# Optimization experiments

Measured on AMD Instinct MI355X. Metric: run time of the kernel, lower is better.

## Reference

```python
import jax, jax.numpy as jnp
import numpy as np

B, DIM, HID = 16384, 1024, 2048


def _ln(x, g, b, eps=1e-5):
    m = x.mean(-1, keepdims=True)
    v = ((x - m) ** 2).mean(-1, keepdims=True)
    return (x - m) / jnp.sqrt(v + eps) * g + b


def _attn1(x_kv, Wv, bv, Wo, bo):
    # seq-len-1 MHA: softmax over a single key is exactly 1 (per head),
    # so output = out_proj(v_proj(kv)); q/k projections cancel identically.
    return (x_kv @ Wv.T + bv) @ Wo.T + bo


def _ffn(x, W1, b1, W2, b2):
    return jnp.maximum(x @ W1.T + b1, 0.0) @ W2.T + b2


def setup_inputs() -> dict:
    key = jax.random.key(0)
    ks = iter(jax.random.split(key, 32))
    s = 0.02
    d = {
        'visual_feat': jax.random.normal(next(ks), (B, DIM), jnp.float32),
        'text_feat': jax.random.normal(next(ks), (B, DIM), jnp.float32),
    }
    for tag in ('sv', 'st', 'v2t', 't2v'):
        d[f'Wv_{tag}'] = jax.random.normal(next(ks), (DIM, DIM), jnp.float32) * s
        d[f'bv_{tag}'] = jnp.zeros((DIM,), jnp.float32)
        d[f'Wo_{tag}'] = jax.random.normal(next(ks), (DIM, DIM), jnp.float32) * s
        d[f'bo_{tag}'] = jnp.zeros((DIM,), jnp.float32)
    for tag in ('v1', 't1', 'v2', 't2'):
        d[f'g_{tag}'] = jnp.ones((DIM,), jnp.float32)
        d[f'be_{tag}'] = jnp.zeros((DIM,), jnp.float32)
    for tag in ('v', 't'):
        d[f'W1_{tag}'] = jax.random.normal(next(ks), (HID, DIM), jnp.float32) * s
        d[f'b1_{tag}'] = jnp.zeros((HID,), jnp.float32)
        d[f'W2_{tag}'] = jax.random.normal(next(ks), (DIM, HID), jnp.float32) * s
        d[f'b2_{tag}'] = jnp.zeros((DIM,), jnp.float32)
    return d


def reference(visual_feat, text_feat,
              Wv_sv, bv_sv, Wo_sv, bo_sv,
              Wv_st, bv_st, Wo_st, bo_st,
              Wv_v2t, bv_v2t, Wo_v2t, bo_v2t,
              Wv_t2v, bv_t2v, Wo_t2v, bo_t2v,
              g_v1, be_v1, g_t1, be_t1, g_v2, be_v2, g_t2, be_t2,
              W1_v, b1_v, W2_v, b2_v, W1_t, b1_t, W2_t, b2_t):
    v_self = _ln(visual_feat + _attn1(visual_feat, Wv_sv, bv_sv, Wo_sv, bo_sv), g_v1, be_v1)
    t_self = _ln(text_feat + _attn1(text_feat, Wv_st, bv_st, Wo_st, bo_st), g_t1, be_t1)
    v_cross = _attn1(t_self, Wv_v2t, bv_v2t, Wo_v2t, bo_v2t)  # v queries t -> depends on kv=t_self only
    t_cross = _attn1(v_self, Wv_t2v, bv_t2v, Wo_t2v, bo_t2v)
    v_fused = _ln(visual_feat + (v_self + v_cross) * 0.5, g_v2, be_v2)
    t_fused = _ln(text_feat + (t_self + t_cross) * 0.5, g_t2, be_t2)
    v_out = v_fused + _ffn(v_fused, W1_v, b1_v, W2_v, b2_v)
    t_out = t_fused + _ffn(t_fused, W1_t, b1_t, W2_t, b2_t)
    new_context = (v_out + t_out) * 0.5
    return (v_out, t_out, new_context)
```

## Files before the change

kernel.cpp:

```cpp
#include <hip/hip_runtime.h>
#include <stdint.h>


typedef unsigned short u16;
typedef __bf16 bf16x8 __attribute__((ext_vector_type(8)));
typedef float f32x4 __attribute__((ext_vector_type(4)));

__device__ __forceinline__ u16 f2bf(float f) {
    uint32_t x = __float_as_uint(f);
    uint32_t r = (x + 0x7fffu + ((x >> 16) & 1u)) >> 16;
    return (u16)r;
}
__device__ __forceinline__ float bf2f(u16 u) {
    return __uint_as_float(((uint32_t)u) << 16);
}

__device__ __forceinline__ void glds16(const u16* g, u16* l) {
    __builtin_amdgcn_global_load_lds(
        (__attribute__((address_space(1))) void*)g,
        (__attribute__((address_space(3))) void*)l, 16, 0, 0);
}

__global__ __launch_bounds__(256) void cvtk(const float* __restrict__ src,
                                            u16* __restrict__ dst) {
    size_t i = ((size_t)blockIdx.x * 256 + threadIdx.x) * 4;
    float4 v = *(const float4*)&src[i];
    ushort4 o;
    o.x = f2bf(v.x); o.y = f2bf(v.y); o.z = f2bf(v.z); o.w = f2bf(v.w);
    *(ushort4*)&dst[i] = o;
}

struct Ptr4 { const float* p[4]; };
__global__ __launch_bounds__(256) void tcvtk(Ptr4 src, u16* __restrict__ dst) {
    __shared__ float t[32][33];
    const int z = blockIdx.z;
    const float* s = src.p[z];
    const int bx = blockIdx.x * 32, by = blockIdx.y * 32;
    const int tx = threadIdx.x & 31, ty = threadIdx.x >> 5;
#pragma unroll
    for (int i = 0; i < 32; i += 8)
        t[ty + i][tx] = s[(size_t)(by + ty + i) * 1024 + bx + tx];
    __syncthreads();
    u16* d = dst + (size_t)z * (1024 * 1024);
#pragma unroll
    for (int i = 0; i < 32; i += 8)
        d[(size_t)(bx + ty + i) * 1024 + by + tx] = f2bf(t[tx][ty + i]);
}

struct BiasArgs { const float* Wo[4]; const float* bv[4]; const float* bo[4]; };
__global__ __launch_bounds__(256) void biask(BiasArgs a, float* __restrict__ out) {
    const int z = blockIdx.y;
    const int row = blockIdx.x * 4 + (threadIdx.x >> 6);
    const int lane = threadIdx.x & 63;
    const float* w = a.Wo[z] + (size_t)row * 1024 + lane * 16;
    const float* v = a.bv[z] + lane * 16;
    float s = 0.f;
#pragma unroll
    for (int i = 0; i < 16; i += 4) {
        float4 w4 = *(const float4*)&w[i];
        float4 v4 = *(const float4*)&v[i];
        s += w4.x * v4.x + w4.y * v4.y + w4.z * v4.z + w4.w * v4.w;
    }
#pragma unroll
    for (int o = 1; o < 64; o <<= 1) s += __shfl_xor(s, o);
    if (lane == 0) out[(size_t)z * 1024 + row] = s + a.bo[z][row];
}

__global__ __launch_bounds__(256) void ctxk(const float* __restrict__ a,
                                            const float* __restrict__ b,
                                            float* __restrict__ o) {
    size_t i = ((size_t)blockIdx.x * 256 + threadIdx.x) * 4;
    float4 va = *(const float4*)&a[i];
    float4 vb = *(const float4*)&b[i];
    float4 vo;
    vo.x = 0.5f * (va.x + vb.x); vo.y = 0.5f * (va.y + vb.y);
    vo.z = 0.5f * (va.z + vb.z); vo.w = 0.5f * (va.w + vb.w);
    *(float4*)&o[i] = vo;
}

__global__ __launch_bounds__(256) void ln_kernel(
    const float* __restrict__ x, const u16* __restrict__ a1,
    const u16* __restrict__ a2, float s,
    const float* __restrict__ g, const float* __restrict__ be,
    u16* __restrict__ out) {
    const int tid = threadIdx.x;
    const size_t base = (size_t)blockIdx.x * 1024;
    const int i0 = tid * 4;

    float4 xv = *(const float4*)&x[base + i0];
    ushort4 u1 = *(const ushort4*)&a1[base + i0];
    float add[4] = {bf2f(u1.x), bf2f(u1.y), bf2f(u1.z), bf2f(u1.w)};
    if (a2) {
        ushort4 u2 = *(const ushort4*)&a2[base + i0];
        add[0] += bf2f(u2.x); add[1] += bf2f(u2.y);
        add[2] += bf2f(u2.z); add[3] += bf2f(u2.w);
    }
    float v[4] = {xv.x, xv.y, xv.z, xv.w};
    float sum = 0.f, ss = 0.f;
#pragma unroll
    for (int j = 0; j < 4; ++j) {
        v[j] += s * add[j];
        sum += v[j];
        ss += v[j] * v[j];
    }
#pragma unroll
    for (int o = 1; o < 64; o <<= 1) {
        sum += __shfl_xor(sum, o);
        ss  += __shfl_xor(ss, o);
    }
    __shared__ float s1[4], s2[4];
    if ((tid & 63) == 0) { s1[tid >> 6] = sum; s2[tid >> 6] = ss; }
    __syncthreads();
    sum = s1[0] + s1[1] + s1[2] + s1[3];
    ss  = s2[0] + s2[1] + s2[2] + s2[3];
    const float mean = sum * (1.f / 1024.f);
    const float var  = ss * (1.f / 1024.f) - mean * mean;
    const float inv  = rsqrtf(var + 1e-5f);

    float4 gv = *(const float4*)&g[i0];
    float4 bv = *(const float4*)&be[i0];
    ushort4 o4;
    o4.x = f2bf((v[0] - mean) * inv * gv.x + bv.x);
    o4.y = f2bf((v[1] - mean) * inv * gv.y + bv.y);
    o4.z = f2bf((v[2] - mean) * inv * gv.z + bv.z);
    o4.w = f2bf((v[3] - mean) * inv * gv.w + bv.w);
    *(ushort4*)&out[base + i0] = o4;
}

__global__ __launch_bounds__(256) void gemm_bt(
    const u16* __restrict__ A, const u16* __restrict__ W,
    const float* __restrict__ bias,
    int M, int N, int K, int mode,
    const u16* __restrict__ resid,
    u16* __restrict__ out_bf, float* __restrict__ out_f,
    size_t sA, size_t sW, size_t sC) {
    __shared__ u16 As[128 * 32];
    __shared__ u16 Bs[128 * 32];

    const int tid  = threadIdx.x;
    const int lane = tid & 63;
    const int wv   = tid >> 6;
    const int wm   = wv >> 1, wn = wv & 1;
    const int M0 = blockIdx.y * 128, N0 = blockIdx.x * 128;
    const int z  = blockIdx.z;
    A += (size_t)z * sA;
    W += (size_t)z * sW;

    const f32x4 fz = {0.f, 0.f, 0.f, 0.f};
    f32x4 acc[4][4];
#pragma unroll
    for (int i = 0; i < 4; ++i)
#pragma unroll
        for (int j = 0; j < 4; ++j) acc[i][j] = fz;

    const int rl = lane >> 2;
    const int gg = (lane & 3) ^ ((lane >> 3) & 3);
    const u16* pA0 = A + (size_t)(M0 + wv * 16 + rl) * K + gg * 8;
    const u16* pA1 = A + (size_t)(M0 + 64 + wv * 16 + rl) * K + gg * 8;
    const u16* pW0 = W + (size_t)(N0 + wv * 16 + rl) * K + gg * 8;
    const u16* pW1 = W + (size_t)(N0 + 64 + wv * 16 + rl) * K + gg * 8;
    u16* ldsA0 = &As[wv * 512];
    u16* ldsA1 = &As[(wv + 4) * 512];
    u16* ldsB0 = &Bs[wv * 512];
    u16* ldsB1 = &Bs[(wv + 4) * 512];

    const int lr  = lane & 15;
    const int q   = lane >> 4;
    const int gsw = ((q ^ ((lr >> 1) & 3)) << 3);

    for (int k0 = 0; k0 < K; k0 += 32) {
        __syncthreads();
        glds16(pA0, ldsA0);
        glds16(pA1, ldsA1);
        glds16(pW0, ldsB0);
        glds16(pW1, ldsB1);
        pA0 += 32; pA1 += 32; pW0 += 32; pW1 += 32;
        __syncthreads();

        bf16x8 af[4], bfr[4];
#pragma unroll
        for (int mi = 0; mi < 4; ++mi)
            af[mi] = *(const bf16x8*)&As[(wm * 64 + mi * 16 + lr) * 32 + gsw];
#pragma unroll
        for (int ni = 0; ni < 4; ++ni)
            bfr[ni] = *(const bf16x8*)&Bs[(wn * 64 + ni * 16 + lr) * 32 + gsw];
#pragma unroll
        for (int mi = 0; mi < 4; ++mi)
#pragma unroll
            for (int ni = 0; ni < 4; ++ni)
                acc[mi][ni] = __builtin_amdgcn_mfma_f32_16x16x32_bf16(
                    af[mi], bfr[ni], acc[mi][ni], 0, 0, 0);
    }

    const int rbase = M0 + wm * 64 + (q << 2);
    const int cbase = N0 + wn * 64 + lr;
    out_bf += (size_t)z * sC;
    out_f  += (size_t)z * sC;
#pragma unroll
    for (int mi = 0; mi < 4; ++mi) {
#pragma unroll
        for (int ni = 0; ni < 4; ++ni) {
            const int c = cbase + ni * 16;
            const float bv = bias ? bias[c] : 0.f;
#pragma unroll
            for (int r = 0; r < 4; ++r) {
                const int rr = rbase + mi * 16 + r;
                float val = acc[mi][ni][r] + bv;
                if (mode == 0) {
                    out_bf[(size_t)rr * N + c] = f2bf(val);
                } else if (mode == 1) {
                    out_bf[(size_t)rr * N + c] = f2bf(val > 0.f ? val : 0.f);
                } else {
                    out_f[(size_t)rr * N + c] =
                        val + bf2f(resid[(size_t)rr * N + c]);
                }
            }
        }
    }
}

extern "C" void kernel_launch(void* const* d_in, const int* in_sizes, int n_in,
                              void* d_out, int out_size, void* d_ws, size_t ws_size,
                              hipStream_t stream) {
    const float* visual = (const float*)d_in[0];
    const float* text   = (const float*)d_in[1];
    const float* Wv_sv  = (const float*)d_in[2];
    const float* bv_sv  = (const float*)d_in[3];
    const float* Wo_sv  = (const float*)d_in[4];
    const float* bo_sv  = (const float*)d_in[5];
    const float* Wv_st  = (const float*)d_in[6];
    const float* bv_st  = (const float*)d_in[7];
    const float* Wo_st  = (const float*)d_in[8];
    const float* bo_st  = (const float*)d_in[9];
    const float* Wv_v2t = (const float*)d_in[10];
    const float* bv_v2t = (const float*)d_in[11];
    const float* Wo_v2t = (const float*)d_in[12];
    const float* bo_v2t = (const float*)d_in[13];
    const float* Wv_t2v = (const float*)d_in[14];
    const float* bv_t2v = (const float*)d_in[15];
    const float* Wo_t2v = (const float*)d_in[16];
    const float* bo_t2v = (const float*)d_in[17];
    const float* g_v1 = (const float*)d_in[18];
    const float* be_v1 = (const float*)d_in[19];
    const float* g_t1 = (const float*)d_in[20];
    const float* be_t1 = (const float*)d_in[21];
    const float* g_v2 = (const float*)d_in[22];
    const float* be_v2 = (const float*)d_in[23];
    const float* g_t2 = (const float*)d_in[24];
    const float* be_t2 = (const float*)d_in[25];
    const float* W1_v = (const float*)d_in[26];
    const float* b1_v = (const float*)d_in[27];
    const float* W2_v = (const float*)d_in[28];
    const float* b2_v = (const float*)d_in[29];
    const float* W1_t = (const float*)d_in[30];
    const float* b1_t = (const float*)d_in[31];
    const float* W2_t = (const float*)d_in[32];
    const float* b2_t = (const float*)d_in[33];

    const int Bsz = 16384, D = 1024, HID = 2048;
    const size_t SQ = (size_t)D * D;
    const size_t BD = (size_t)Bsz * D;

    u16* wb = (u16*)d_ws;
    u16* wWc   = wb + 0 * SQ;
    u16* wW1_v = wb + 4 * SQ;
    u16* wW2_v = wb + 6 * SQ;
    u16* wW1_t = wb + 8 * SQ;
    u16* wW2_t = wb + 10 * SQ;
    float* bcAll = (float*)(wb + 12 * SQ);
    u16* P0 = wb + 13 * SQ;
    u16* P1 = wb + 29 * SQ;
    u16* P2 = wb + 45 * SQ;
    u16* P3 = wb + 61 * SQ;
    u16* Hbuf = P0;
    u16* wWo  = P3;
    u16* wWvT = P3 + 4 * SQ;

    float* out0 = (float*)d_out;
    float* out1 = out0 + BD;
    float* out2 = out0 + 2 * BD;

    auto cvt = [&](const float* src, u16* dst, size_t n) {
        cvtk<<<dim3((unsigned)(n / 1024)), dim3(256), 0, stream>>>(src, dst);
    };
    auto gemm = [&](const u16* A, const u16* W, const float* bias, int M, int N,
                    int K, int mode, const u16* resid, void* out, int zdim,
                    size_t sA, size_t sW, size_t sC) {
        dim3 grid((unsigned)(N / 128), (unsigned)(M / 128), (unsigned)zdim);
        gemm_bt<<<grid, dim3(256), 0, stream>>>(A, W, bias, M, N, K, mode,
                                                resid, (u16*)out, (float*)out,
                                                sA, sW, sC);
    };
    auto ln = [&](const float* x, const u16* a1, const u16* a2, float s,
                  const float* g, const float* be, u16* out) {
        ln_kernel<<<dim3(Bsz), dim3(256), 0, stream>>>(x, a1, a2, s, g, be, out);
    };

    cvt(Wo_sv, wWo + 0 * SQ, SQ);
    cvt(Wo_st, wWo + 1 * SQ, SQ);
    cvt(Wo_v2t, wWo + 2 * SQ, SQ);
    cvt(Wo_t2v, wWo + 3 * SQ, SQ);
    Ptr4 wvp = {{Wv_sv, Wv_st, Wv_v2t, Wv_t2v}};
    tcvtk<<<dim3(32, 32, 4), dim3(256), 0, stream>>>(wvp, wWvT);
    cvt(W1_v, wW1_v, 2 * SQ); cvt(W2_v, wW2_v, 2 * SQ);
    cvt(W1_t, wW1_t, 2 * SQ); cvt(W2_t, wW2_t, 2 * SQ);

    gemm(wWo, wWvT, nullptr, D, D, D, 0, nullptr, wWc, 4, SQ, SQ, SQ);
    BiasArgs ba = {{Wo_sv, Wo_st, Wo_v2t, Wo_t2v},
                   {bv_sv, bv_st, bv_v2t, bv_t2v},
                   {bo_sv, bo_st, bo_v2t, bo_t2v}};
    biask<<<dim3(256, 4), dim3(256), 0, stream>>>(ba, bcAll);
    const float* bc_sv  = bcAll;
    const float* bc_st  = bcAll + 1024;
    const float* bc_v2t = bcAll + 2048;
    const float* bc_t2v = bcAll + 3072;

    cvt(visual, P0, BD);
    gemm(P0, wWc + 0 * SQ, bc_sv, Bsz, D, D, 0, nullptr, P1, 1, 0, 0, 0);
    ln(visual, P1, nullptr, 1.f, g_v1, be_v1, P1);
    cvt(text, P0, BD);
    gemm(P0, wWc + 1 * SQ, bc_st, Bsz, D, D, 0, nullptr, P2, 1, 0, 0, 0);
    ln(text, P2, nullptr, 1.f, g_t1, be_t1, P2);

    gemm(P2, wWc + 2 * SQ, bc_v2t, Bsz, D, D, 0, nullptr, P0, 1, 0, 0, 0);
    ln(visual, P1, P0, 0.5f, g_v2, be_v2, P3);
    gemm(P1, wWc + 3 * SQ, bc_t2v, Bsz, D, D, 0, nullptr, P0, 1, 0, 0, 0);
    ln(text, P2, P0, 0.5f, g_t2, be_t2, P2);

    gemm(P3, wW1_v, b1_v, Bsz, HID, D, 1, nullptr, Hbuf, 1, 0, 0, 0);
    gemm(Hbuf, wW2_v, b2_v, Bsz, D, HID, 2, P3, out0, 1, 0, 0, 0);
    gemm(P2, wW1_t, b1_t, Bsz, HID, D, 1, nullptr, Hbuf, 1, 0, 0, 0);
    gemm(Hbuf, wW2_t, b2_t, Bsz, D, HID, 2, P2, out1, 1, 0, 0, 0);

    ctxk<<<dim3((unsigned)(BD / 1024)), dim3(256), 0, stream>>>(out0, out1, out2);
}
```

Baseline: 1.372 ms.

## Replace 128x128 GEMM with double-buffered 256x256 tile kernel and XCD remap

Replaces the 128x128, 256-thread bf16 GEMM with a 256x256 tile computed by 512 threads, using a K-step of 64 and double-buffered LDS. Global-to-LDS loads for the next tiles are interleaved with MFMA phases under explicit barriers, waitcnts and setprio. Workgroup ids are remapped so consecutive tiles share an XCD for L2 locality. Larger tiles raise arithmetic intensity and overlap loads with compute, at the cost of about 128KB LDS per block, higher register pressure, and fewer blocks when M or N is small.

```diff
diff --git a/kernel.cpp b/kernel.cpp
--- a/kernel.cpp
+++ b/kernel.cpp
@@ -127,92 +127,151 @@
     *(ushort4*)&out[base + i0] = o4;
 }
 
-__global__ __launch_bounds__(256) void gemm_bt(
+#define GBAR()  asm volatile("s_barrier" ::: "memory")
+#define LGKM0() asm volatile("s_waitcnt lgkmcnt(0)" ::: "memory")
+
+#define PH_READ_A(mi0)                                                        \
+    a0[0] = *(const bf16x8*)&LDS[b][0][0][arow + (mi0) * 512];                \
+    a0[1] = *(const bf16x8*)&LDS[b][0][1][arow + (mi0) * 512];                \
+    a1[0] = *(const bf16x8*)&LDS[b][0][0][arow + ((mi0) + 1) * 512];          \
+    a1[1] = *(const bf16x8*)&LDS[b][0][1][arow + ((mi0) + 1) * 512];
+
+#define PH_MFMA(mi0)                                                          \
+    __builtin_amdgcn_s_setprio(1);                                            \
+    _Pragma("unroll")                                                         \
+    for (int ni = 0; ni < 4; ++ni) {                                          \
+        acc[mi0][ni] = __builtin_amdgcn_mfma_f32_16x16x32_bf16(               \
+            a0[0], bF[ni][0], acc[mi0][ni], 0, 0, 0);                         \
+        acc[mi0][ni] = __builtin_amdgcn_mfma_f32_16x16x32_bf16(               \
+            a0[1], bF[ni][1], acc[mi0][ni], 0, 0, 0);                         \
+        acc[(mi0) + 1][ni] = __builtin_amdgcn_mfma_f32_16x16x32_bf16(         \
+            a1[0], bF[ni][0], acc[(mi0) + 1][ni], 0, 0, 0);                   \
+        acc[(mi0) + 1][ni] = __builtin_amdgcn_mfma_f32_16x16x32_bf16(         \
+            a1[1], bF[ni][1], acc[(mi0) + 1][ni], 0, 0, 0);                   \
+    }                                                                         \
+    __builtin_amdgcn_s_setprio(0);
+
+__global__ __launch_bounds__(512, 2) void gemm256(
     const u16* __restrict__ A, const u16* __restrict__ W,
     const float* __restrict__ bias,
     int M, int N, int K, int mode,
     const u16* __restrict__ resid,
     u16* __restrict__ out_bf, float* __restrict__ out_f,
     size_t sA, size_t sW, size_t sC) {
-    __shared__ u16 As[128 * 32];
-    __shared__ u16 Bs[128 * 32];
+    __shared__ u16 LDS[2][2][2][8192];
 
     const int tid  = threadIdx.x;
     const int lane = tid & 63;
     const int wv   = tid >> 6;
-    const int wm   = wv >> 1, wn = wv & 1;
-    const int M0 = blockIdx.y * 128, N0 = blockIdx.x * 128;
-    const int z  = blockIdx.z;
+    const int wm   = wv >> 2, wn = wv & 3;
+
+    const int gx   = gridDim.x;
+    const int nwg  = gx * gridDim.y;
+    const int orig = blockIdx.y * gx + blockIdx.x;
+    const int qq = nwg >> 3, rr = nwg & 7;
+    const int xcd = orig & 7, loc = orig >> 3;
+    const int wgid =
+        (xcd < rr ? xcd * (qq + 1) : rr * (qq + 1) + (xcd - rr) * qq) + loc;
+    const int M0 = (wgid / gx) * 256, N0 = (wgid % gx) * 256;
+
+    const int z = blockIdx.z;
     A += (size_t)z * sA;
     W += (size_t)z * sW;
 
     const f32x4 fz = {0.f, 0.f, 0.f, 0.f};
-    f32x4 acc[4][4];
-#pragma unroll
-    for (int i = 0; i < 4; ++i)
+    f32x4 acc[8][4];
+#pragma unroll
+    for (int i = 0; i < 8; ++i)
 #pragma unroll
         for (int j = 0; j < 4; ++j) acc[i][j] = fz;
 
     const int rl = lane >> 2;
-    const int gg = (lane & 3) ^ ((lane >> 3) & 3);
-    const u16* pA0 = A + (size_t)(M0 + wv * 16 + rl) * K + gg * 8;
-    const u16* pA1 = A + (size_t)(M0 + 64 + wv * 16 + rl) * K + gg * 8;
-    const u16* pW0 = W + (size_t)(N0 + wv * 16 + rl) * K + gg * 8;
-    const u16* pW1 = W + (size_t)(N0 + 64 + wv * 16 + rl) * K + gg * 8;
-    u16* ldsA0 = &As[wv * 512];
-    u16* ldsA1 = &As[(wv + 4) * 512];
-    u16* ldsB0 = &Bs[wv * 512];
-    u16* ldsB1 = &Bs[(wv + 4) * 512];
-
-    const int lr  = lane & 15;
-    const int q   = lane >> 4;
-    const int gsw = ((q ^ ((lr >> 1) & 3)) << 3);
-
-    for (int k0 = 0; k0 < K; k0 += 32) {
-        __syncthreads();
-        glds16(pA0, ldsA0);
-        glds16(pA1, ldsA1);
-        glds16(pW0, ldsB0);
-        glds16(pW1, ldsB1);
-        pA0 += 32; pA1 += 32; pW0 += 32; pW1 += 32;
-        __syncthreads();
-
-        bf16x8 af[4], bfr[4];
-#pragma unroll
-        for (int mi = 0; mi < 4; ++mi)
-            af[mi] = *(const bf16x8*)&As[(wm * 64 + mi * 16 + lr) * 32 + gsw];
-#pragma unroll
-        for (int ni = 0; ni < 4; ++ni)
-            bfr[ni] = *(const bf16x8*)&Bs[(wn * 64 + ni * 16 + lr) * 32 + gsw];
-#pragma unroll
-        for (int mi = 0; mi < 4; ++mi)
-#pragma unroll
-            for (int ni = 0; ni < 4; ++ni)
-                acc[mi][ni] = __builtin_amdgcn_mfma_f32_16x16x32_bf16(
-                    af[mi], bfr[ni], acc[mi][ni], 0, 0, 0);
-    }
-
-    const int rbase = M0 + wm * 64 + (q << 2);
-    const int cbase = N0 + wn * 64 + lr;
+    const int gS = (lane & 3) ^ ((lane >> 3) & 3);
+    const u16* aS = A + (size_t)(M0 + wv * 32 + rl) * K + gS * 8;
+    const u16* bS = W + (size_t)(N0 + wv * 32 + rl) * K + gS * 8;
+    const size_t cstep = (size_t)16 * K;
+
+    const int lr = lane & 15, qf = lane >> 4;
+    const int fsw  = ((qf ^ ((lr >> 1) & 3)) << 3);
+    const int arow = (wm * 128 + lr) * 32 + fsw;
+    const int brow = (wn * 64 + lr) * 32 + fsw;
+
+    const int nt = K >> 6;
+
+    auto STAGE = [&](int mat, int t, int kh) {
+        const u16* src = (mat ? bS : aS) + t * 64 + kh * 32;
+        u16* dst = &LDS[t & 1][mat][kh][wv * 1024];
+        glds16(src, dst);
+        glds16(src + cstep, dst + 512);
+    };
+
+    STAGE(0, 0, 0); STAGE(0, 0, 1);
+    STAGE(1, 0, 0); STAGE(1, 0, 1);
+    if (nt > 1) {
+        STAGE(1, 1, 0); STAGE(1, 1, 1);
+        asm volatile("s_waitcnt vmcnt(4)" ::: "memory");
+    } else {
+        asm volatile("s_waitcnt vmcnt(0)" ::: "memory");
+    }
+    GBAR();
+
+    for (int t = 0; t < nt; ++t) {
+        const int b = t & 1;
+        bf16x8 bF[4][2], a0[2], a1[2];
+
+        PH_READ_A(0);
+#pragma unroll
+        for (int ni = 0; ni < 4; ++ni) {
+            bF[ni][0] = *(const bf16x8*)&LDS[b][1][0][brow + ni * 512];
+            bF[ni][1] = *(const bf16x8*)&LDS[b][1][1][brow + ni * 512];
+        }
+        if (t + 1 < nt) STAGE(0, t + 1, 0);
+        GBAR(); LGKM0();
+        PH_MFMA(0);
+        GBAR();
+
+        PH_READ_A(2);
+        if (t + 1 < nt) STAGE(0, t + 1, 1);
+        GBAR(); LGKM0();
+        PH_MFMA(2);
+        GBAR();
+
+        PH_READ_A(4);
+        if (t + 2 < nt) STAGE(1, t + 2, 0);
+        GBAR(); LGKM0();
+        PH_MFMA(4);
+        GBAR();
+
+        PH_READ_A(6);
+        if (t + 2 < nt) STAGE(1, t + 2, 1);
+        GBAR(); LGKM0();
+        PH_MFMA(6);
+        if (t + 2 < nt) asm volatile("s_waitcnt vmcnt(4)" ::: "memory");
+        else            asm volatile("s_waitcnt vmcnt(0)" ::: "memory");
+        GBAR();
+    }
+
+    const int rb = M0 + wm * 128 + (qf << 2);
+    const int cb = N0 + wn * 64 + lr;
     out_bf += (size_t)z * sC;
     out_f  += (size_t)z * sC;
 #pragma unroll
-    for (int mi = 0; mi < 4; ++mi) {
+    for (int mi = 0; mi < 8; ++mi) {
 #pragma unroll
         for (int ni = 0; ni < 4; ++ni) {
-            const int c = cbase + ni * 16;
+            const int c = cb + ni * 16;
             const float bv = bias ? bias[c] : 0.f;
 #pragma unroll
             for (int r = 0; r < 4; ++r) {
-                const int rr = rbase + mi * 16 + r;
+                const int rrw = rb + mi * 16 + r;
                 float val = acc[mi][ni][r] + bv;
                 if (mode == 0) {
-                    out_bf[(size_t)rr * N + c] = f2bf(val);
+                    out_bf[(size_t)rrw * N + c] = f2bf(val);
                 } else if (mode == 1) {
-                    out_bf[(size_t)rr * N + c] = f2bf(val > 0.f ? val : 0.f);
+                    out_bf[(size_t)rrw * N + c] = f2bf(val > 0.f ? val : 0.f);
                 } else {
-                    out_f[(size_t)rr * N + c] =
-                        val + bf2f(resid[(size_t)rr * N + c]);
+                    out_f[(size_t)rrw * N + c] =
+                        val + bf2f(resid[(size_t)rrw * N + c]);
                 }
             }
         }
@@ -283,11 +342,11 @@
     auto cvt = [&](const float* src, u16* dst, size_t n) {
         cvtk<<<dim3((unsigned)(n / 1024)), dim3(256), 0, stream>>>(src, dst);
     };
-    auto gemm = [&](const u16* A, const u16* W, const float* bias, int M, int N,
-                    int K, int mode, const u16* resid, void* out, int zdim,
-                    size_t sA, size_t sW, size_t sC) {
-        dim3 grid((unsigned)(N / 128), (unsigned)(M / 128), (unsigned)zdim);
-        gemm_bt<<<grid, dim3(256), 0, stream>>>(A, W, bias, M, N, K, mode,
+    auto gemm = [&](const u16* Am, const u16* Wm, const float* bias, int M,
+                    int N, int K, int mode, const u16* resid, void* out,
+                    int zdim, size_t sA, size_t sW, size_t sC) {
+        dim3 grid((unsigned)(N / 256), (unsigned)(M / 256), (unsigned)zdim);
+        gemm256<<<grid, dim3(512), 0, stream>>>(Am, Wm, bias, M, N, K, mode,
                                                 resid, (u16*)out, (float*)out,
                                                 sA, sW, sC);
     };
```

Result: faster. 1.122 ms (-18.3%).
